# Kernel optimization log

Hardware: AMD Instinct MI355X
Metric: run time of the kernel (lower is better)

## Reference

```python
import jax, jax.numpy as jnp
import numpy as np

B, WIN, DM, DG, K = 32, 128, 1024, 64, 15  # batch, win_size(node feat dim), d_model(#nodes), graph embed, top_k


def setup_inputs() -> dict:
    key = jax.random.key(0)
    ks = jax.random.split(key, 7)
    sc_in = 1.0 / np.sqrt(WIN)
    return {
        "x": jax.random.normal(ks[0], (B, WIN, DM), jnp.float32),
        "Wq": jax.random.normal(ks[1], (DG, WIN), jnp.float32) * sc_in,
        "bq": jax.random.normal(ks[2], (DG,), jnp.float32) * 0.02,
        "Wk": jax.random.normal(ks[3], (DG, WIN), jnp.float32) * sc_in,
        "bk": jax.random.normal(ks[4], (DG,), jnp.float32) * 0.02,
        "Wg": jax.random.normal(ks[5], (WIN, WIN), jnp.float32) * sc_in,  # GCNConv lin weight [out,in]
        "bg": jax.random.normal(ks[6], (WIN,), jnp.float32) * 0.02,
    }


def _gcn_one(nf, Wq, bq, Wk, bk, Wg, bg):
    # nf: [N, F] node features (N = d_model, F = win_size)
    N = nf.shape[0]
    q = nf @ Wq.T + bq                      # [N, DG]
    k = nf @ Wk.T + bk                      # [N, DG]
    scores = (q @ k.T) * (1.0 / np.sqrt(DG))  # [N, N]
    scores = jnp.where(jnp.eye(N, dtype=bool), -jnp.inf, scores)
    _, tgt = jax.lax.top_k(scores, K)       # [N, K] top-k neighbors per source node
    src = jnp.repeat(jnp.arange(N), K)      # [N*K]
    tgt = tgt.reshape(-1)                   # [N*K]
    loops = jnp.arange(N)
    # manual self loops (module) + self loops added internally by GCNConv (default add_self_loops=True)
    src_all = jnp.concatenate([src, loops, loops])
    tgt_all = jnp.concatenate([tgt, loops, loops])
    # gcn_norm: degree over target (col) with unit edge weights
    deg = jax.ops.segment_sum(jnp.ones_like(tgt_all, jnp.float32), tgt_all, num_segments=N)
    dinv = jnp.where(deg > 0, jax.lax.rsqrt(deg), 0.0)
    norm = dinv[src_all] * dinv[tgt_all]    # [E]
    h = nf @ Wg.T                           # [N, F] linear transform (no bias inside lin)
    msg = h[src_all] * norm[:, None]        # gather + scale
    out = jax.ops.segment_sum(msg, tgt_all, num_segments=N) + bg  # scatter-add + bias
    return out                              # [N, F]


def reference(x, Wq, bq, Wk, bk, Wg, bg):
    # x: [B, win_size, d_model] -> nodes: [B, d_model, win_size]
    nodes = x.transpose(0, 2, 1)
    h = jax.vmap(lambda nf: _gcn_one(nf, Wq, bq, Wk, bk, Wg, bg))(nodes)  # [B, N, F]
    # n_layers == 1: no ReLU/dropout applied after last layer
    return h.transpose(0, 2, 1)  # [B, win_size, d_model]
```

## Files before the change

kernel.cpp:

```cpp
#include <hip/hip_runtime.h>

#define NBATCH 32
#define NN     1024
#define NF     128
#define NDG    64
#define TOPK   15

#define OFF_QH    ((size_t)0)
#define OFF_QL    ((size_t)4194304)
#define OFF_KH    ((size_t)8388608)
#define OFF_KL    ((size_t)12582912)
#define OFF_H     ((size_t)16777216)
#define OFF_DEG   ((size_t)33554432)
#define OFF_BMP   ((size_t)33685504)
#define OFF_WL    ((size_t)37879808)
#define OFF_TOPK  ((size_t)38010880)
#define OFF_W64   ((size_t)40108032)
#define OFF_QT64  ((size_t)40239104)
#define OFF_KT64  ((size_t)57016320)
#define OFF_TMP   ((size_t)0)

typedef short s8v  __attribute__((ext_vector_type(8)));
typedef float f4v  __attribute__((ext_vector_type(4)));
typedef unsigned short us8v __attribute__((ext_vector_type(8)));

__device__ inline unsigned short bf16_rne(float f) {
    unsigned u = __float_as_uint(f);
    return (unsigned short)((u + 0x7FFFu + ((u >> 16) & 1u)) >> 16);
}
__device__ inline float bf16_tof(unsigned short h) { return __uint_as_float(((unsigned)h) << 16); }

__device__ inline unsigned pack22(float s) {
    unsigned u   = __float_as_uint(s);
    int      mag = (int)(u & 0x7FFFFFFFu);
    int      t   = mag - 0x38800000;
    t = t < 0 ? 0 : (t > 0x07FFFFFF ? 0x07FFFFFF : t);
    unsigned ts = (unsigned)t >> 6;
    return ((int)u < 0) ? (0x1FFFFFu - ts) : (0x200000u | ts);
}
__device__ inline float dec22(unsigned val22) {
    bool pos = (val22 & 0x200000u) != 0;
    unsigned ts = pos ? (val22 & 0x1FFFFFu) : (0x1FFFFFu - (val22 & 0x1FFFFFu));
    float f = __uint_as_float((ts << 6) + 0x38800000u);
    return pos ? f : -f;
}

__global__ __launch_bounds__(256) void k_upcast(const float* __restrict__ Wq,
                                                const float* __restrict__ Wk,
                                                double* __restrict__ Wq64,
                                                double* __restrict__ Wk64) {
    int i = blockIdx.x * 256 + threadIdx.x;
    Wq64[i] = (double)Wq[i];
    Wk64[i] = (double)Wk[i];
}

__global__ __launch_bounds__(256) void k_prep(
    const float* __restrict__ x, const float* __restrict__ bq, const float* __restrict__ bk,
    const double* __restrict__ Wq64, const double* __restrict__ Wk64,
    const float* __restrict__ Wg,
    unsigned short* __restrict__ qh, unsigned short* __restrict__ ql,
    unsigned short* __restrict__ kh, unsigned short* __restrict__ kl,
    double* __restrict__ qT64, double* __restrict__ kT64,
    float* __restrict__ h,
    uint4* __restrict__ zbase, int zn)
{
    __shared__ float xs[64 * 129];
    const int t = threadIdx.x;
    const int l = t & 63;
    const int w = t >> 6;
    const int uw = __builtin_amdgcn_readfirstlane(w);
    const int bid = blockIdx.x;
    const int lid = (bid & 7) * 128 + (bid >> 3);
    const int b    = lid >> 5;
    const int half = (lid >> 4) & 1;
    const int n0   = (lid & 15) * 64;

    {
        int lid0 = bid * 256 + t;
        for (int i = lid0; i < zn; i += 262144)
            zbase[i] = make_uint4(0u, 0u, 0u, 0u);
    }

    {
        const int j = t & 63, fg = t >> 6;
        for (int ff = 0; ff < 32; ++ff) {
            int f = fg + ff * 4;
            xs[j * 129 + f] = x[((size_t)b * NF + f) * NN + n0 + j];
        }
    }
    __syncthreads();

    {
        const int d0 = half * 32 + uw * 8;
        double accq[8], acck[8];
        #pragma unroll
        for (int dd = 0; dd < 8; ++dd) {
            accq[dd] = (double)bq[d0 + dd];
            acck[dd] = (double)bk[d0 + dd];
        }
        for (int fc = 0; fc < 32; ++fc) {
            double dx0 = (double)xs[l * 129 + fc * 4 + 0];
            double dx1 = (double)xs[l * 129 + fc * 4 + 1];
            double dx2 = (double)xs[l * 129 + fc * 4 + 2];
            double dx3 = (double)xs[l * 129 + fc * 4 + 3];
            #pragma unroll
            for (int dd = 0; dd < 8; ++dd) {
                int d = d0 + dd;
                const double* wq = &Wq64[d * NF + fc * 4];
                const double* wk = &Wk64[d * NF + fc * 4];
                accq[dd] += dx0 * wq[0] + dx1 * wq[1] + dx2 * wq[2] + dx3 * wq[3];
                acck[dd] += dx0 * wk[0] + dx1 * wk[1] + dx2 * wk[2] + dx3 * wk[3];
            }
        }
        #pragma unroll
        for (int dd = 0; dd < 8; ++dd) {
            size_t idx = ((size_t)b * NDG + d0 + dd) * NN + n0 + l;
            qT64[idx] = accq[dd];
            kT64[idx] = acck[dd];
        }
        us8v qh0, ql0, kh0, kl0;
        #pragma unroll
        for (int dd = 0; dd < 8; ++dd) {
            float fq = (float)accq[dd];
            unsigned short h1 = bf16_rne(fq);
            unsigned short l1 = bf16_rne(fq - bf16_tof(h1));
            float fk = (float)acck[dd];
            unsigned short h2 = bf16_rne(fk);
            unsigned short l2 = bf16_rne(fk - bf16_tof(h2));
            qh0[dd] = h1; ql0[dd] = l1; kh0[dd] = h2; kl0[dd] = l2;
        }
        size_t nb = ((size_t)b * NN + n0 + l) * NDG + d0;
        *(us8v*)&qh[nb] = qh0;
        *(us8v*)&ql[nb] = ql0;
        *(us8v*)&kh[nb] = kh0;
        *(us8v*)&kl[nb] = kl0;
    }

    {
        const int fp0 = half * 64 + uw * 16;
        float acc[16];
        #pragma unroll
        for (int i = 0; i < 16; ++i) acc[i] = 0.f;
        for (int fc = 0; fc < 32; ++fc) {
            float x0 = xs[l * 129 + fc * 4 + 0];
            float x1 = xs[l * 129 + fc * 4 + 1];
            float x2 = xs[l * 129 + fc * 4 + 2];
            float x3 = xs[l * 129 + fc * 4 + 3];
            #pragma unroll
            for (int ff = 0; ff < 16; ++ff) {
                const float* wg = &Wg[(fp0 + ff) * NF + fc * 4];
                acc[ff] += x0 * wg[0] + x1 * wg[1] + x2 * wg[2] + x3 * wg[3];
            }
        }
        __syncthreads();
        #pragma unroll
        for (int ff = 0; ff < 16; ++ff) xs[l * 129 + fp0 + ff] = acc[ff];
        __syncthreads();
        for (int r = 0; r < 16; ++r) {
            int idx = t + 256 * r;
            int n = idx >> 6, f = idx & 63;
            h[((size_t)b * NN + n0 + n) * NF + half * 64 + f] = xs[n * 129 + half * 64 + f];
        }
    }
}

__device__ inline void bsort64_2(unsigned& va, unsigned& vb, int l) {
    #pragma unroll
    for (int k = 2; k <= 64; k <<= 1) {
        #pragma unroll
        for (int j = k >> 1; j >= 1; j >>= 1) {
            unsigned pa = (unsigned)__shfl_xor((int)va, j, 64);
            unsigned pb = (unsigned)__shfl_xor((int)vb, j, 64);
            bool tm = ((l & k) == 0) == ((l & j) == 0);
            unsigned ha = va > pa ? va : pa, la = va > pa ? pa : va;
            unsigned hb = vb > pb ? vb : pb, lb = vb > pb ? pb : vb;
            va = tm ? ha : la;
            vb = tm ? hb : lb;
        }
    }
}

__global__ __launch_bounds__(256) void k_score(
    const unsigned short* __restrict__ qh, const unsigned short* __restrict__ ql,
    const unsigned short* __restrict__ kh, const unsigned short* __restrict__ kl,
    const float* __restrict__ bk,
    unsigned int* __restrict__ bmp,
    int* __restrict__ topk, int* __restrict__ wl_cnt, int* __restrict__ wl)
{
    __shared__ unsigned slots[32 * 96];
    __shared__ int      cntw[32 * 4];
    const int t = threadIdx.x, l = t & 63, w = t >> 6;
    const int bid = blockIdx.x;
    const int lid = (bid & 7) * 128 + (bid >> 3);
    const int b = lid >> 5, row0 = (lid & 31) * 32;
    const int m = l & 15, q4 = l >> 4;

    s8v ah0[2], ah1[2], al0[2], al1[2];
    #pragma unroll
    for (int g = 0; g < 2; ++g) {
        size_t abase = ((size_t)b * NN + row0 + g * 16 + m) * NDG + q4 * 8;
        ah0[g] = *(const s8v*)&qh[abase];
        ah1[g] = *(const s8v*)&qh[abase + 32];
        al0[g] = *(const s8v*)&ql[abase];
        al1[g] = *(const s8v*)&ql[abase + 32];
    }

    unsigned Trow[2][4];
    #pragma unroll
    for (int g = 0; g < 2; ++g) {
        float ssq = 0.f, smn = 0.f;
        #pragma unroll
        for (int j = 0; j < 8; ++j) {
            float q0 = bf16_tof(((us8v)ah0[g])[j]) + bf16_tof(((us8v)al0[g])[j]);
            float q1 = bf16_tof(((us8v)ah1[g])[j]) + bf16_tof(((us8v)al1[g])[j]);
            float b0 = bk[q4 * 8 + j];
            float b1 = bk[q4 * 8 + 32 + j];
            ssq += q0 * q0 + q1 * q1;
            smn += q0 * b0 + q1 * b1;
        }
        ssq += __shfl_xor(ssq, 16, 64); ssq += __shfl_xor(ssq, 32, 64);
        smn += __shfl_xor(smn, 16, 64); smn += __shfl_xor(smn, 32, 64);
        float t_m = 0.125f * smn + 0.2250f * __builtin_sqrtf(ssq);
        unsigned Tm = pack22(t_m) << 10;
        #pragma unroll
        for (int r = 0; r < 4; ++r)
            Trow[g][r] = (unsigned)__shfl((int)Tm, 4 * q4 + r, 64);
    }

    const int colbase = w * 256;
    int basec[2][4] = {{0,0,0,0},{0,0,0,0}};

    s8v Bh0[2], Bh1[2], Bl0[2], Bl1[2];
    {
        size_t bb = ((size_t)b * NN + colbase + m) * NDG + q4 * 8;
        Bh0[0] = *(const s8v*)&kh[bb];
        Bh1[0] = *(const s8v*)&kh[bb + 32];
        Bl0[0] = *(const s8v*)&kl[bb];
        Bl1[0] = *(const s8v*)&kl[bb + 32];
    }
    #pragma unroll
    for (int tt = 0; tt < 16; ++tt) {
        const int cur = tt & 1;
        if (tt < 15) {
            size_t bb = ((size_t)b * NN + colbase + (tt + 1) * 16 + m) * NDG + q4 * 8;
            Bh0[cur ^ 1] = *(const s8v*)&kh[bb];
            Bh1[cur ^ 1] = *(const s8v*)&kh[bb + 32];
            Bl0[cur ^ 1] = *(const s8v*)&kl[bb];
            Bl1[cur ^ 1] = *(const s8v*)&kl[bb + 32];
        }
        const int col = colbase + tt * 16 + m;
        #pragma unroll
        for (int g = 0; g < 2; ++g) {
            f4v acc = {0.f, 0.f, 0.f, 0.f};
            acc = __builtin_amdgcn_mfma_f32_16x16x32_bf16(al0[g], Bl0[cur], acc, 0, 0, 0);
            acc = __builtin_amdgcn_mfma_f32_16x16x32_bf16(al1[g], Bl1[cur], acc, 0, 0, 0);
            acc = __builtin_amdgcn_mfma_f32_16x16x32_bf16(ah0[g], Bl0[cur], acc, 0, 0, 0);
            acc = __builtin_amdgcn_mfma_f32_16x16x32_bf16(ah1[g], Bl1[cur], acc, 0, 0, 0);
            acc = __builtin_amdgcn_mfma_f32_16x16x32_bf16(al0[g], Bh0[cur], acc, 0, 0, 0);
            acc = __builtin_amdgcn_mfma_f32_16x16x32_bf16(al1[g], Bh1[cur], acc, 0, 0, 0);
            acc = __builtin_amdgcn_mfma_f32_16x16x32_bf16(ah0[g], Bh0[cur], acc, 0, 0, 0);
            acc = __builtin_amdgcn_mfma_f32_16x16x32_bf16(ah1[g], Bh1[cur], acc, 0, 0, 0);
            #pragma unroll
            for (int r = 0; r < 4; ++r) {
                const int rloc = g * 16 + q4 * 4 + r;
                const int grow = row0 + rloc;
                float s = acc[r] * 0.125f;
                unsigned c22 = (col == grow) ? 0u : pack22(s);
                unsigned v = (c22 << 10) | (unsigned)(1023 - col);
                bool p = v >= Trow[g][r];
                unsigned long long mk = __ballot(p);
                unsigned w16 = (unsigned)(mk >> (q4 * 16)) & 0xFFFFu;
                int idx = basec[g][r] + __popc(w16 & ((1u << m) - 1u));
                if (p && idx < 24) slots[rloc * 96 + w * 24 + idx] = v;
                basec[g][r] += __popc(w16);
            }
        }
    }
    if (m == 0) {
        #pragma unroll
        for (int g = 0; g < 2; ++g)
            #pragma unroll
            for (int r = 0; r < 4; ++r)
                cntw[(g * 16 + q4 * 4 + r) * 4 + w] = basec[g][r];
    }
    __syncthreads();

    #pragma unroll
    for (int pp = 0; pp < 4; ++pp) {
        const int rA = w * 8 + 2 * pp, rB = rA + 1;
        int a0 = cntw[rA * 4 + 0], a1 = cntw[rA * 4 + 1], a2 = cntw[rA * 4 + 2], a3 = cntw[rA * 4 + 3];
        int b0 = cntw[rB * 4 + 0], b1 = cntw[rB * 4 + 1], b2 = cntw[rB * 4 + 2], b3 = cntw[rB * 4 + 3];
        bool ovA = (a0 > 24) || (a1 > 24) || (a2 > 24) || (a3 > 24);
        bool ovB = (b0 > 24) || (b1 > 24) || (b2 > 24) || (b3 > 24);
        int rawA = a0 + a1 + a2 + a3, rawB = b0 + b1 + b2 + b3;
        a0 = a0 > 24 ? 24 : a0; a1 = a1 > 24 ? 24 : a1; a2 = a2 > 24 ? 24 : a2; a3 = a3 > 24 ? 24 : a3;
        b0 = b0 > 24 ? 24 : b0; b1 = b1 > 24 ? 24 : b1; b2 = b2 > 24 ? 24 : b2; b3 = b3 > 24 ? 24 : b3;
        int PA1 = a0, PA2 = a0 + a1, PA3 = a0 + a1 + a2, CA = PA3 + a3;
        int PB1 = b0, PB2 = b0 + b1, PB3 = b0 + b1 + b2, CB = PB3 + b3;
        bool fbA = ovA || rawA < 16 || rawA > 64;
        bool fbB = ovB || rawB < 16 || rawB > 64;

        int jA = (l >= PA1) + (l >= PA2) + (l >= PA3);
        int jB = (l >= PB1) + (l >= PB2) + (l >= PB3);
        int baseA = jA == 0 ? 0 : (jA == 1 ? PA1 : (jA == 2 ? PA2 : PA3));
        int baseB = jB == 0 ? 0 : (jB == 1 ? PB1 : (jB == 2 ? PB2 : PB3));
        unsigned cva = (l < CA) ? slots[rA * 96 + jA * 24 + (l - baseA)] : 0u;
        unsigned cvb = (l < CB) ? slots[rB * 96 + jB * 24 + (l - baseB)] : 0u;
        bsort64_2(cva, cvb, l);

        #pragma unroll
        for (int rr = 0; rr < 2; ++rr) {
            const int grow = row0 + (rr == 0 ? rA : rB);
            unsigned res   = rr == 0 ? cva : cvb;
            const bool fb  = rr == 0 ? fbA : fbB;

            unsigned r14 = (unsigned)__shfl((int)res, 14, 64);
            unsigned r15 = (unsigned)__shfl((int)res, 15, 64);
            bool flagged;
            if (fb) {
                flagged = true;
            } else {
                float s15 = dec22(r14 >> 10), s16 = dec22(r15 >> 10);
                unsigned e15 = (__float_as_uint(fabsf(s15)) >> 23) & 255u;
                unsigned e16 = (__float_as_uint(fabsf(s16)) >> 23) & 255u;
                unsigned e = e15 > e16 ? e15 : e16;
                float qq = __uint_as_float((e - 17) << 23);
                flagged = (s15 - s16) < (4.f * qq + 1e-4f);
            }
            if (l < 15) {
                int col = fb ? ((grow + 1 + l) & 1023)
                             : (1023 - (int)(res & 1023u));
                atomicOr(&bmp[((size_t)b * NN + col) * 32 + (grow >> 5)], 1u << (grow & 31));
                if (flagged) topk[(b * NN + grow) * 16 + l] = col;
            }
            if (l == 0 && flagged) {
                int idx = atomicAdd(wl_cnt, 1);
                if (idx < 32767) wl[idx] = b * NN + grow;
            }
        }
    }
}

__global__ __launch_bounds__(256) void k_repair(
    const double* __restrict__ qT64, const double* __restrict__ kT64,
    const int* __restrict__ topk, const int* __restrict__ wl_cnt, const int* __restrict__ wl,
    unsigned int* __restrict__ bmp)
{
    const int t = threadIdx.x, l = t & 63, w = t >> 6;
    __shared__ double qld[64];
    __shared__ double cmax[4];
    __shared__ int    cidx[4];
    __shared__ int    oldset[15], newset[15];
    const double NEGINF = -__builtin_inf();
    int n = wl_cnt[0]; if (n > 32767) n = 32767;

    for (int i = blockIdx.x; i < n; i += 1024) {
        int rg = wl[i];
        int b = rg >> 10, row = rg & 1023;

        __syncthreads();
        if (t < 64) qld[t] = qT64[((size_t)b * NDG + t) * NN + row];
        if (t < 15) oldset[t] = topk[(b * NN + row) * 16 + t];
        __syncthreads();

        const double* kb = &kT64[(size_t)b * NDG * NN];
        const int base = l + 256 * w;
        const int c0 = base, c1 = base + 64, c2 = base + 128, c3 = base + 192;
        double s0 = 0.0, s1 = 0.0, s2 = 0.0, s3 = 0.0;
        double b0 = kb[c0], b1 = kb[c1], b2 = kb[c2], b3 = kb[c3];
        for (int d = 0; d < 64; ++d) {
            double n0, n1, n2, n3;
            if (d < 63) {
                const double* kr = kb + (size_t)(d + 1) * NN;
                n0 = kr[c0]; n1 = kr[c1]; n2 = kr[c2]; n3 = kr[c3];
            }
            double qd = qld[d];
            s0 += qd * b0; s1 += qd * b1; s2 += qd * b2; s3 += qd * b3;
            if (d < 63) { b0 = n0; b1 = n1; b2 = n2; b3 = n3; }
        }
        if (c0 == row) s0 = NEGINF;
        if (c1 == row) s1 = NEGINF;
        if (c2 == row) s2 = NEGINF;
        if (c3 == row) s3 = NEGINF;

        for (int it = 0; it < 15; ++it) {
            double lv = NEGINF; int lc = 0x7fffffff;
            if (s0 > lv) { lv = s0; lc = c0; }
            if (s1 > lv) { lv = s1; lc = c1; }
            if (s2 > lv) { lv = s2; lc = c2; }
            if (s3 > lv) { lv = s3; lc = c3; }
            #pragma unroll
            for (int off = 1; off < 64; off <<= 1) {
                double ov = __shfl_xor(lv, off, 64);
                int    oc = __shfl_xor(lc, off, 64);
                if (ov > lv || (ov == lv && oc < lc)) { lv = ov; lc = oc; }
            }
            if (l == 0) { cmax[w] = lv; cidx[w] = lc; }
            __syncthreads();
            if (t == 0) {
                double bv = cmax[0]; int bc = cidx[0];
                #pragma unroll
                for (int ww = 1; ww < 4; ++ww)
                    if (cmax[ww] > bv || (cmax[ww] == bv && cidx[ww] < bc)) { bv = cmax[ww]; bc = cidx[ww]; }
                newset[it] = bc;
            }
            __syncthreads();
            int bc = newset[it];
            if (c0 == bc) s0 = NEGINF;
            if (c1 == bc) s1 = NEGINF;
            if (c2 == bc) s2 = NEGINF;
            if (c3 == bc) s3 = NEGINF;
        }

        if (t < 15) {
            int cn = newset[t];
            bool found = false;
            #pragma unroll
            for (int j = 0; j < 15; ++j) found = found || (oldset[j] == cn);
            if (!found)
                atomicOr(&bmp[((size_t)b * NN + cn) * 32 + (row >> 5)], 1u << (row & 31));
            int co = oldset[t];
            found = false;
            #pragma unroll
            for (int j = 0; j < 15; ++j) found = found || (newset[j] == co);
            if (!found)
                atomicAnd(&bmp[((size_t)b * NN + co) * 32 + (row >> 5)], ~(1u << (row & 31)));
        }
    }
}

__global__ __launch_bounds__(256) void k_deg(const unsigned int* __restrict__ bmp,
                                             int* __restrict__ deg)
{
    int i = blockIdx.x * 256 + threadIdx.x;
    const uint4* p = (const uint4*)(bmp + (size_t)i * 32);
    int s = 0;
    #pragma unroll
    for (int j = 0; j < 8; ++j) {
        uint4 v = p[j];
        s += __popc(v.x) + __popc(v.y) + __popc(v.z) + __popc(v.w);
    }
    deg[i] = s;
}

__global__ __launch_bounds__(128) void k_gather(
    const float* __restrict__ h, const float* __restrict__ bg,
    const int* __restrict__ deg, const unsigned int* __restrict__ bmp,
    float* __restrict__ tmp)
{
    __shared__ int list[1024];
    __shared__ float nrm[1024];
    __shared__ int scnt;
    const int bid = blockIdx.x;
    const int lid = (bid & 7) * 4096 + (bid >> 3);
    const int b = lid >> 10, tgt = lid & 1023;
    const int t = threadIdx.x;
    if (t < 32) {
        unsigned word = bmp[((size_t)b * NN + tgt) * 32 + t];
        int pc = __popc(word);
        int pre = pc;
        #pragma unroll
        for (int d = 1; d < 32; d <<= 1) {
            int o = __shfl_up(pre, d, 32);
            if (t >= d) pre += o;
        }
        if (t == 31) scnt = pre;
        int idx = pre - pc;
        while (word) {
            int s = __ffs(word) - 1;
            word &= word - 1;
            list[idx++] = t * 32 + s;
        }
    }
    __syncthreads();
    const int cnt = scnt;
    for (int e = t; e < cnt; e += 128)
        nrm[e] = rsqrtf((float)(deg[b * NN + list[e]] + 2));
    __syncthreads();
    const int f = t;
    float dt = rsqrtf((float)(deg[b * NN + tgt] + 2));
    float a0 = 0.f, a1 = 0.f, a2 = 0.f, a3 = 0.f;
    int e = 0;
    for (; e + 4 <= cnt; e += 4) {
        a0 += h[((size_t)b * NN + list[e + 0]) * NF + f] * nrm[e + 0];
        a1 += h[((size_t)b * NN + list[e + 1]) * NF + f] * nrm[e + 1];
        a2 += h[((size_t)b * NN + list[e + 2]) * NF + f] * nrm[e + 2];
        a3 += h[((size_t)b * NN + list[e + 3]) * NF + f] * nrm[e + 3];
    }
    for (; e < cnt; ++e)
        a0 += h[((size_t)b * NN + list[e]) * NF + f] * nrm[e];
    float acc = 2.0f * dt * h[((size_t)b * NN + tgt) * NF + f] + ((a0 + a1) + (a2 + a3));
    tmp[((size_t)b * NN + tgt) * NF + f] = bg[f] + dt * acc;
}

__global__ __launch_bounds__(256) void k_transpose(const float* __restrict__ tmp,
                                                   float* __restrict__ out)
{
    __shared__ float tile[32][33];
    const int t = threadIdx.x;
    const int n0 = blockIdx.x * 32, f0 = blockIdx.y * 32, b = blockIdx.z;
    const int c = t & 31, rb = t >> 5;
    #pragma unroll
    for (int i = 0; i < 4; ++i) {
        int r = rb + i * 8;
        tile[r][c] = tmp[((size_t)b * NN + n0 + r) * NF + f0 + c];
    }
    __syncthreads();
    #pragma unroll
    for (int i = 0; i < 4; ++i) {
        int r = rb + i * 8;
        out[((size_t)b * NF + f0 + r) * NN + n0 + c] = tile[c][r];
    }
}

extern "C" void kernel_launch(void* const* d_in, const int* in_sizes, int n_in,
                              void* d_out, int out_size, void* d_ws, size_t ws_size,
                              hipStream_t stream)
{
    const float* x  = (const float*)d_in[0];
    const float* Wq = (const float*)d_in[1];
    const float* bq = (const float*)d_in[2];
    const float* Wk = (const float*)d_in[3];
    const float* bk = (const float*)d_in[4];
    const float* Wg = (const float*)d_in[5];
    const float* bg = (const float*)d_in[6];
    float* out = (float*)d_out;
    char* ws = (char*)d_ws;

    unsigned short* qh = (unsigned short*)(ws + OFF_QH);
    unsigned short* ql = (unsigned short*)(ws + OFF_QL);
    unsigned short* kh = (unsigned short*)(ws + OFF_KH);
    unsigned short* kl = (unsigned short*)(ws + OFF_KL);
    float*          h   = (float*)(ws + OFF_H);
    int*            deg = (int*)(ws + OFF_DEG);
    unsigned int*   bmp = (unsigned int*)(ws + OFF_BMP);
    int*            wlc = (int*)(ws + OFF_WL);
    int*            wl  = wlc + 1;
    int*            tpk = (int*)(ws + OFF_TOPK);
    double*         Wq64 = (double*)(ws + OFF_W64);
    double*         Wk64 = Wq64 + 8192;
    double*         qT64 = (double*)(ws + OFF_QT64);
    double*         kT64 = (double*)(ws + OFF_KT64);
    float*          tmp  = (float*)(ws + OFF_TMP);

    k_upcast<<<32, 256, 0, stream>>>(Wq, Wk, Wq64, Wk64);
    k_prep<<<1024, 256, 0, stream>>>(x, bq, bk, Wq64, Wk64, Wg,
                                     qh, ql, kh, kl, qT64, kT64, h,
                                     (uint4*)(ws + OFF_DEG), 270337);
    k_score<<<1024, 256, 0, stream>>>(qh, ql, kh, kl, bk, bmp, tpk, wlc, wl);
    k_repair<<<1024, 256, 0, stream>>>(qT64, kT64, tpk, wlc, wl, bmp);
    k_deg<<<128, 256, 0, stream>>>(bmp, deg);
    k_gather<<<32768, 128, 0, stream>>>(h, bg, deg, bmp, tmp);
    k_transpose<<<dim3(32, 4, 32), 256, 0, stream>>>(tmp, out);
}
```

Measured before the change: 271.5 us.

## Drop fp64 projections in prep; recompute q in repair, store k as fp32

The q/k projections in the prep kernel now accumulate in fp32 instead of fp64, which removes the weight upcast kernel and the large fp64 qT/kT buffers. Only k is written back, as fp32 in transposed form. The repair kernel recomputes the q row in fp64 from x for each flagged row and reads the fp32 k. The score kernel's threshold test now compares raw fp32 scores and only packs candidates that pass. The cost is lower precision in the repair path and in the q/k splits, which may change tie-breaking or top-k selection.

```diff
diff --git a/kernel.cpp b/kernel.cpp
--- a/kernel.cpp
+++ b/kernel.cpp
@@ -15,9 +15,7 @@
 #define OFF_BMP   ((size_t)33685504)
 #define OFF_WL    ((size_t)37879808)
 #define OFF_TOPK  ((size_t)38010880)
-#define OFF_W64   ((size_t)40108032)
-#define OFF_QT64  ((size_t)40239104)
-#define OFF_KT64  ((size_t)57016320)
+#define OFF_KT32  ((size_t)40239104)
 #define OFF_TMP   ((size_t)0)
 
 typedef short s8v  __attribute__((ext_vector_type(8)));
@@ -45,22 +43,13 @@
     return pos ? f : -f;
 }
 
-__global__ __launch_bounds__(256) void k_upcast(const float* __restrict__ Wq,
-                                                const float* __restrict__ Wk,
-                                                double* __restrict__ Wq64,
-                                                double* __restrict__ Wk64) {
-    int i = blockIdx.x * 256 + threadIdx.x;
-    Wq64[i] = (double)Wq[i];
-    Wk64[i] = (double)Wk[i];
-}
-
 __global__ __launch_bounds__(256) void k_prep(
     const float* __restrict__ x, const float* __restrict__ bq, const float* __restrict__ bk,
-    const double* __restrict__ Wq64, const double* __restrict__ Wk64,
+    const float* __restrict__ Wq, const float* __restrict__ Wk,
     const float* __restrict__ Wg,
     unsigned short* __restrict__ qh, unsigned short* __restrict__ ql,
     unsigned short* __restrict__ kh, unsigned short* __restrict__ kl,
-    double* __restrict__ qT64, double* __restrict__ kT64,
+    float* __restrict__ kT32,
     float* __restrict__ h,
     uint4* __restrict__ zbase, int zn)
 {
@@ -92,41 +81,36 @@
 
     {
         const int d0 = half * 32 + uw * 8;
-        double accq[8], acck[8];
+        float accq[8], acck[8];
         #pragma unroll
         for (int dd = 0; dd < 8; ++dd) {
-            accq[dd] = (double)bq[d0 + dd];
-            acck[dd] = (double)bk[d0 + dd];
+            accq[dd] = bq[d0 + dd];
+            acck[dd] = bk[d0 + dd];
         }
         for (int fc = 0; fc < 32; ++fc) {
-            double dx0 = (double)xs[l * 129 + fc * 4 + 0];
-            double dx1 = (double)xs[l * 129 + fc * 4 + 1];
-            double dx2 = (double)xs[l * 129 + fc * 4 + 2];
-            double dx3 = (double)xs[l * 129 + fc * 4 + 3];
+            float x0 = xs[l * 129 + fc * 4 + 0];
+            float x1 = xs[l * 129 + fc * 4 + 1];
+            float x2 = xs[l * 129 + fc * 4 + 2];
+            float x3 = xs[l * 129 + fc * 4 + 3];
             #pragma unroll
             for (int dd = 0; dd < 8; ++dd) {
                 int d = d0 + dd;
-                const double* wq = &Wq64[d * NF + fc * 4];
-                const double* wk = &Wk64[d * NF + fc * 4];
-                accq[dd] += dx0 * wq[0] + dx1 * wq[1] + dx2 * wq[2] + dx3 * wq[3];
-                acck[dd] += dx0 * wk[0] + dx1 * wk[1] + dx2 * wk[2] + dx3 * wk[3];
-            }
-        }
+                const float* wq = &Wq[d * NF + fc * 4];
+                const float* wk = &Wk[d * NF + fc * 4];
+                accq[dd] += x0 * wq[0] + x1 * wq[1] + x2 * wq[2] + x3 * wq[3];
+                acck[dd] += x0 * wk[0] + x1 * wk[1] + x2 * wk[2] + x3 * wk[3];
+            }
+        }
+        #pragma unroll
+        for (int dd = 0; dd < 8; ++dd)
+            kT32[((size_t)b * NDG + d0 + dd) * NN + n0 + l] = acck[dd];
+        us8v qh0, ql0, kh0, kl0;
         #pragma unroll
         for (int dd = 0; dd < 8; ++dd) {
-            size_t idx = ((size_t)b * NDG + d0 + dd) * NN + n0 + l;
-            qT64[idx] = accq[dd];
-            kT64[idx] = acck[dd];
-        }
-        us8v qh0, ql0, kh0, kl0;
-        #pragma unroll
-        for (int dd = 0; dd < 8; ++dd) {
-            float fq = (float)accq[dd];
-            unsigned short h1 = bf16_rne(fq);
-            unsigned short l1 = bf16_rne(fq - bf16_tof(h1));
-            float fk = (float)acck[dd];
-            unsigned short h2 = bf16_rne(fk);
-            unsigned short l2 = bf16_rne(fk - bf16_tof(h2));
+            unsigned short h1 = bf16_rne(accq[dd]);
+            unsigned short l1 = bf16_rne(accq[dd] - bf16_tof(h1));
+            unsigned short h2 = bf16_rne(acck[dd]);
+            unsigned short l2 = bf16_rne(acck[dd] - bf16_tof(h2));
             qh0[dd] = h1; ql0[dd] = l1; kh0[dd] = h2; kl0[dd] = l2;
         }
         size_t nb = ((size_t)b * NN + n0 + l) * NDG + d0;
@@ -205,7 +189,7 @@
         al1[g] = *(const s8v*)&ql[abase + 32];
     }
 
-    unsigned Trow[2][4];
+    float Tr[2][4];
     #pragma unroll
     for (int g = 0; g < 2; ++g) {
         float ssq = 0.f, smn = 0.f;
@@ -220,11 +204,10 @@
         }
         ssq += __shfl_xor(ssq, 16, 64); ssq += __shfl_xor(ssq, 32, 64);
         smn += __shfl_xor(smn, 16, 64); smn += __shfl_xor(smn, 32, 64);
-        float t_m = 0.125f * smn + 0.2250f * __builtin_sqrtf(ssq);
-        unsigned Tm = pack22(t_m) << 10;
+        float t8 = smn + 1.8f * __builtin_sqrtf(ssq);
         #pragma unroll
         for (int r = 0; r < 4; ++r)
-            Trow[g][r] = (unsigned)__shfl((int)Tm, 4 * q4 + r, 64);
+            Tr[g][r] = __shfl(t8, 4 * q4 + r, 64);
     }
 
     const int colbase = w * 256;
@@ -264,14 +247,14 @@
             for (int r = 0; r < 4; ++r) {
                 const int rloc = g * 16 + q4 * 4 + r;
                 const int grow = row0 + rloc;
-                float s = acc[r] * 0.125f;
-                unsigned c22 = (col == grow) ? 0u : pack22(s);
-                unsigned v = (c22 << 10) | (unsigned)(1023 - col);
-                bool p = v >= Trow[g][r];
+                bool p = (acc[r] >= Tr[g][r]) && (col != grow);
                 unsigned long long mk = __ballot(p);
                 unsigned w16 = (unsigned)(mk >> (q4 * 16)) & 0xFFFFu;
                 int idx = basec[g][r] + __popc(w16 & ((1u << m) - 1u));
-                if (p && idx < 24) slots[rloc * 96 + w * 24 + idx] = v;
+                if (p && idx < 24) {
+                    float s = acc[r] * 0.125f;
+                    slots[rloc * 96 + w * 24 + idx] = (pack22(s) << 10) | (unsigned)(1023 - col);
+                }
                 basec[g][r] += __popc(w16);
             }
         }
@@ -342,11 +325,13 @@
 }
 
 __global__ __launch_bounds__(256) void k_repair(
-    const double* __restrict__ qT64, const double* __restrict__ kT64,
+    const float* __restrict__ x, const float* __restrict__ bq, const float* __restrict__ Wq,
+    const float* __restrict__ kT32,
     const int* __restrict__ topk, const int* __restrict__ wl_cnt, const int* __restrict__ wl,
     unsigned int* __restrict__ bmp)
 {
     const int t = threadIdx.x, l = t & 63, w = t >> 6;
+    __shared__ float  xrow[128];
     __shared__ double qld[64];
     __shared__ double cmax[4];
     __shared__ int    cidx[4];
@@ -359,23 +344,32 @@
         int b = rg >> 10, row = rg & 1023;
 
         __syncthreads();
-        if (t < 64) qld[t] = qT64[((size_t)b * NDG + t) * NN + row];
+        if (t < 128) xrow[t] = x[((size_t)b * NF + t) * NN + row];
         if (t < 15) oldset[t] = topk[(b * NN + row) * 16 + t];
         __syncthreads();
-
-        const double* kb = &kT64[(size_t)b * NDG * NN];
+        if (t < 64) {
+            double acc = (double)bq[t];
+            const float* wq = &Wq[t * NF];
+            for (int f = 0; f < 128; ++f)
+                acc += (double)xrow[f] * (double)wq[f];
+            qld[t] = acc;
+        }
+        __syncthreads();
+
+        const float* kb = &kT32[(size_t)b * NDG * NN];
         const int base = l + 256 * w;
         const int c0 = base, c1 = base + 64, c2 = base + 128, c3 = base + 192;
         double s0 = 0.0, s1 = 0.0, s2 = 0.0, s3 = 0.0;
-        double b0 = kb[c0], b1 = kb[c1], b2 = kb[c2], b3 = kb[c3];
+        float b0 = kb[c0], b1 = kb[c1], b2 = kb[c2], b3 = kb[c3];
         for (int d = 0; d < 64; ++d) {
-            double n0, n1, n2, n3;
+            float n0, n1, n2, n3;
             if (d < 63) {
-                const double* kr = kb + (size_t)(d + 1) * NN;
+                const float* kr = kb + (size_t)(d + 1) * NN;
                 n0 = kr[c0]; n1 = kr[c1]; n2 = kr[c2]; n3 = kr[c3];
             }
             double qd = qld[d];
-            s0 += qd * b0; s1 += qd * b1; s2 += qd * b2; s3 += qd * b3;
+            s0 += qd * (double)b0; s1 += qd * (double)b1;
+            s2 += qd * (double)b2; s3 += qd * (double)b3;
             if (d < 63) { b0 = n0; b1 = n1; b2 = n2; b3 = n3; }
         }
         if (c0 == row) s0 = NEGINF;
@@ -537,18 +531,14 @@
     int*            wlc = (int*)(ws + OFF_WL);
     int*            wl  = wlc + 1;
     int*            tpk = (int*)(ws + OFF_TOPK);
-    double*         Wq64 = (double*)(ws + OFF_W64);
-    double*         Wk64 = Wq64 + 8192;
-    double*         qT64 = (double*)(ws + OFF_QT64);
-    double*         kT64 = (double*)(ws + OFF_KT64);
+    float*          kT32 = (float*)(ws + OFF_KT32);
     float*          tmp  = (float*)(ws + OFF_TMP);
 
-    k_upcast<<<32, 256, 0, stream>>>(Wq, Wk, Wq64, Wk64);
-    k_prep<<<1024, 256, 0, stream>>>(x, bq, bk, Wq64, Wk64, Wg,
-                                     qh, ql, kh, kl, qT64, kT64, h,
+    k_prep<<<1024, 256, 0, stream>>>(x, bq, bk, Wq, Wk, Wg,
+                                     qh, ql, kh, kl, kT32, h,
                                      (uint4*)(ws + OFF_DEG), 270337);
     k_score<<<1024, 256, 0, stream>>>(qh, ql, kh, kl, bk, bmp, tpk, wlc, wl);
-    k_repair<<<1024, 256, 0, stream>>>(qT64, kT64, tpk, wlc, wl, bmp);
+    k_repair<<<1024, 256, 0, stream>>>(x, bq, Wq, kT32, tpk, wlc, wl, bmp);
     k_deg<<<128, 256, 0, stream>>>(bmp, deg);
     k_gather<<<32768, 128, 0, stream>>>(h, bg, deg, bmp, tmp);
     k_transpose<<<dim3(32, 4, 32), 256, 0, stream>>>(tmp, out);
```

Measured after the change: 257.5 us. 1.05x faster.
